# Optimization experiments

Measured on AMD Instinct MI355X. Metric: run time of the kernel, lower is better.

Reference implementation:

```python
import jax, jax.numpy as jnp
import numpy as np

B, T, C = 2, 2048, 2048
N_HEAD, N_KV, HEAD_DIM = 32, 8, 64
REPEATS = N_HEAD // N_KV
WINDOW = 1024
ROPE_BASE = 10000.0


def setup_inputs() -> dict:
    key = jax.random.key(0)
    ks = jax.random.split(key, 5)
    s = 0.02
    return {
        "x": jax.random.normal(ks[0], (B, T, C), jnp.float32),
        "Wq": jax.random.normal(ks[1], (C, N_HEAD * HEAD_DIM), jnp.float32) * s,
        "Wk": jax.random.normal(ks[2], (C, N_KV * HEAD_DIM), jnp.float32) * s,
        "Wv": jax.random.normal(ks[3], (C, N_KV * HEAD_DIM), jnp.float32) * s,
        "Wo": jax.random.normal(ks[4], (N_HEAD * HEAD_DIM, C), jnp.float32) * s,
    }


def _rope(q, k):
    # q: (B,H,T,D), k: (B,Hk,T,D) -- standard rotate-half RoPE
    D = q.shape[-1]
    inv_freq = 1.0 / (ROPE_BASE ** (jnp.arange(0, D, 2, dtype=jnp.float32) / D))
    ang = jnp.arange(q.shape[2], dtype=jnp.float32)[:, None] * inv_freq[None, :]  # (T, D/2)
    cos = jnp.concatenate([jnp.cos(ang), jnp.cos(ang)], axis=-1)  # (T, D)
    sin = jnp.concatenate([jnp.sin(ang), jnp.sin(ang)], axis=-1)

    def rot_half(x):
        x1, x2 = jnp.split(x, 2, axis=-1)
        return jnp.concatenate([-x2, x1], axis=-1)

    def apply(x):
        return x * cos + rot_half(x) * sin

    return apply(q), apply(k)


def reference(x, Wq, Wk, Wv, Wo):
    Bx, Tx, Cx = x.shape
    q = (x @ Wq).reshape(Bx, Tx, N_HEAD, HEAD_DIM).transpose(0, 2, 1, 3)   # (B,H,T,D)
    k = (x @ Wk).reshape(Bx, Tx, N_KV, HEAD_DIM).transpose(0, 2, 1, 3)     # (B,Hk,T,D)
    v = (x @ Wv).reshape(Bx, Tx, N_KV, HEAD_DIM).transpose(0, 2, 1, 3)
    q, k = _rope(q, k)

    # GQA: group queries per kv head instead of repeat_interleave on k/v (same math)
    qg = q.reshape(Bx, N_KV, REPEATS, Tx, HEAD_DIM)
    scale = 1.0 / jnp.sqrt(jnp.float32(HEAD_DIM))
    scores = jnp.einsum('bgrtd,bgsd->bgrts', qg, k) * scale  # (B,Hk,rep,T,T)

    # sliding-window causal mask: attend to j <= i and i - j < WINDOW
    i = jnp.arange(Tx)[:, None]
    j = jnp.arange(Tx)[None, :]
    allowed = (j <= i) & (i - j < WINDOW)
    scores = jnp.where(allowed, scores, -jnp.inf)

    attn = jax.nn.softmax(scores.astype(jnp.float32), axis=-1).astype(q.dtype)
    out = jnp.einsum('bgrts,bgsd->bgrtd', attn, v)            # (B,Hk,rep,T,D)
    out = out.reshape(Bx, N_HEAD, Tx, HEAD_DIM).transpose(0, 2, 1, 3).reshape(Bx, Tx, N_HEAD * HEAD_DIM)
    return out @ Wo
```

## Files before the change

kernel.cpp:

```cpp
#include <hip/hip_runtime.h>

typedef unsigned short u16;
typedef __attribute__((ext_vector_type(8))) unsigned short u16x8;
typedef __attribute__((ext_vector_type(2))) unsigned int u32x2;
typedef __attribute__((ext_vector_type(8))) __bf16 bf16x8;
typedef __attribute__((ext_vector_type(4))) float f32x4;

#define T_SEQ 2048
#define WINDOW 1024
#define QSCALE 0.18033688011112042f

static __device__ __forceinline__ u16 f2bf(float f) {
    unsigned int u = __float_as_uint(f);
    u += 0x7fffu + ((u >> 16) & 1u);
    return (u16)(u >> 16);
}
static __device__ __forceinline__ float bf2f(u16 h) {
    return __uint_as_float(((unsigned int)h) << 16);
}
static __device__ __forceinline__ bf16x8 ld_bf8(const u16* p) {
    return __builtin_bit_cast(bf16x8, *(const u16x8*)p);
}
static __device__ __forceinline__ unsigned int cvt_pk_bf16(float lo, float hi) {
    unsigned int r;
    asm("v_cvt_pk_bf16_f32 %0, %1, %2" : "=v"(r) : "v"(lo), "v"(hi));
    return r;
}
static __device__ __forceinline__ float exp2f_raw(float x) {
#if __has_builtin(__builtin_amdgcn_exp2f)
    return __builtin_amdgcn_exp2f(x);
#else
    return exp2f(x);
#endif
}
static __device__ __forceinline__ void g2l16(const void* g, void* l) {
    __builtin_amdgcn_global_load_lds(
        (const __attribute__((address_space(1))) void*)g,
        (__attribute__((address_space(3))) void*)l, 16, 0, 0);
}

__global__ __launch_bounds__(256)
void rope_tab_kernel(float2* __restrict__ tab)
{
    int idx = blockIdx.x * 256 + threadIdx.x;
    int t = idx >> 5, dp = idx & 31;
    float inv_freq = __expf(-dp * 0.28782313662425574f);
    float ang = (float)t * inv_freq;
    float s, c;
    sincosf(ang, &s, &c);
    tab[idx] = make_float2(c, s);
}

__global__ __launch_bounds__(256)
void convert_x(const float* __restrict__ src, u16* __restrict__ dst)
{
    int i8 = blockIdx.x * 256 + threadIdx.x;
    size_t base = (size_t)i8 * 8;
    float4 a = *(const float4*)(src + base);
    float4 b = *(const float4*)(src + base + 4);
    u16x8 o = { f2bf(a.x), f2bf(a.y), f2bf(a.z), f2bf(a.w),
                f2bf(b.x), f2bf(b.y), f2bf(b.z), f2bf(b.w) };
    *(u16x8*)(dst + base) = o;
}

__global__ __launch_bounds__(256)
void trans_conv_all(const float* __restrict__ Wq, const float* __restrict__ Wk,
                    const float* __restrict__ Wv, const float* __restrict__ Wo,
                    u16* __restrict__ WqkvT, u16* __restrict__ WoT)
{
    __shared__ __align__(16) u16 tile[64][72];
    const int z = blockIdx.z;
    const float* src; int N; float scale; u16* dst;
    if (z == 0)      { src = Wq; N = 2048; scale = QSCALE; dst = WqkvT; }
    else if (z == 1) { src = Wk; N = 512;  scale = 1.f;    dst = WqkvT + (size_t)2048 * 2048; }
    else if (z == 2) { src = Wv; N = 512;  scale = 1.f;    dst = WqkvT + (size_t)2560 * 2048; }
    else             { src = Wo; N = 2048; scale = 1.f;    dst = WoT; }
    if ((int)blockIdx.y * 64 >= N) return;

    const int tid = threadIdx.x;
    const int k0 = blockIdx.x * 64;
    const int n0 = blockIdx.y * 64;
    {
        int r = tid >> 2, c0 = (tid & 3) * 16;
        const float* sp = src + (size_t)(k0 + r) * N + n0 + c0;
        float4 v0 = *(const float4*)(sp + 0);
        float4 v1 = *(const float4*)(sp + 4);
        float4 v2 = *(const float4*)(sp + 8);
        float4 v3 = *(const float4*)(sp + 12);
        u16x8 s0 = { f2bf(v0.x * scale), f2bf(v0.y * scale), f2bf(v0.z * scale), f2bf(v0.w * scale),
                     f2bf(v1.x * scale), f2bf(v1.y * scale), f2bf(v1.z * scale), f2bf(v1.w * scale) };
        u16x8 s1 = { f2bf(v2.x * scale), f2bf(v2.y * scale), f2bf(v2.z * scale), f2bf(v2.w * scale),
                     f2bf(v3.x * scale), f2bf(v3.y * scale), f2bf(v3.z * scale), f2bf(v3.w * scale) };
        *(u16x8*)&tile[r][c0]     = s0;
        *(u16x8*)&tile[r][c0 + 8] = s1;
    }
    __syncthreads();
    {
        int n = tid >> 2, j0 = (tid & 3) * 16;
        u16x8 o0, o1;
        #pragma unroll
        for (int i = 0; i < 8; ++i) o0[i] = tile[j0 + i][n];
        #pragma unroll
        for (int i = 0; i < 8; ++i) o1[i] = tile[j0 + 8 + i][n];
        u16* dp = dst + (size_t)(n0 + n) * 2048 + k0 + j0;
        *(u16x8*)dp       = o0;
        *(u16x8*)(dp + 8) = o1;
    }
}

struct GemmAcc { f32x4 a[8][4]; };

__device__ __forceinline__ void gemm_core_128(const u16* __restrict__ Ag,
                                              const u16* __restrict__ Bg,
                                              u16 (*Al)[64], u16 (*Bl)[64],
                                              int lane, int w, GemmAcc& acc)
{
    const int r8 = lane >> 3;
    const int cs = (lane & 7) ^ r8;
    const u16* ag = Ag + (size_t)(w * 64 + r8) * 2048 + cs * 8;
    const u16* bg = Bg + (size_t)(w * 64 + r8) * 2048 + cs * 8;
    const int fr = lane & 15;
    const int hq = lane >> 4;

    for (int kb = 0; kb < 2048; kb += 64) {
        #pragma unroll
        for (int ii = 0; ii < 8; ++ii)
            g2l16(ag + (size_t)(ii * 8) * 2048 + kb, &Al[w * 64 + ii * 8][0]);
        #pragma unroll
        for (int ii = 0; ii < 8; ++ii)
            g2l16(bg + (size_t)(ii * 8) * 2048 + kb, &Bl[w * 64 + ii * 8][0]);
        __syncthreads();

        #pragma unroll
        for (int kk = 0; kk < 2; ++kk) {
            bf16x8 af[8], bfn[4];
            #pragma unroll
            for (int m = 0; m < 8; ++m) {
                int row = m * 16 + fr;
                int pc = (kk * 4 + hq) ^ (row & 7);
                af[m] = ld_bf8(&Al[row][pc * 8]);
            }
            #pragma unroll
            for (int n = 0; n < 4; ++n) {
                int row = w * 64 + n * 16 + fr;
                int pc = (kk * 4 + hq) ^ (row & 7);
                bfn[n] = ld_bf8(&Bl[row][pc * 8]);
            }
            #pragma unroll
            for (int m = 0; m < 8; ++m)
                #pragma unroll
                for (int n = 0; n < 4; ++n)
                    acc.a[m][n] = __builtin_amdgcn_mfma_f32_16x16x32_bf16(af[m], bfn[n], acc.a[m][n], 0, 0, 0);
        }
        __syncthreads();
    }
}

__global__ __launch_bounds__(128, 2)
void qkv_gemm(const u16* __restrict__ xb, const u16* __restrict__ Wt,
              const float2* __restrict__ tab,
              u16* __restrict__ Qb, u16* __restrict__ Kb, u16* __restrict__ Vb)
{
    __shared__ __align__(16) u16 Al[128][64];
    __shared__ __align__(16) u16 Bl[128][64];
    const int tid = threadIdx.x;
    const int lane = tid & 63;
    const int w = tid >> 6;
    const int m0  = blockIdx.x * 128;
    const int n0g = blockIdx.y * 128;

    GemmAcc acc = {};
    gemm_core_128(xb + (size_t)m0 * 2048, Wt + (size_t)n0g * 2048, Al, Bl, lane, w, acc);

    const int hq = lane >> 4;
    const int c0 = lane & 15;
    const int colbase = n0g + w * 64;
    const bool isV = (n0g >= 2560);
    const bool isQ = (n0g < 2048);

    #pragma unroll
    for (int m = 0; m < 8; ++m) {
        #pragma unroll
        for (int r = 0; r < 4; ++r) {
            int rw = m0 + m * 16 + hq * 4 + r;
            int b = rw >> 11, t = rw & 2047;
            if (!isV) {
                #pragma unroll
                for (int np = 0; np < 2; ++np) {
                    int dp = np * 16 + c0;
                    float2 cs = tab[t * 32 + dp];
                    float x1 = acc.a[m][np][r];
                    float x2 = acc.a[m][np + 2][r];
                    float lo = x1 * cs.x - x2 * cs.y;
                    float hi = x2 * cs.x + x1 * cs.y;
                    if (isQ) {
                        int h = colbase >> 6;
                        size_t base = (((size_t)b * 32 + h) * 2048 + t) * 64 + dp;
                        Qb[base]      = f2bf(lo);
                        Qb[base + 32] = f2bf(hi);
                    } else {
                        int hk = (colbase - 2048) >> 6;
                        size_t base = (((size_t)b * 8 + hk) * 2048 + t) * 64 + dp;
                        Kb[base]      = f2bf(lo);
                        Kb[base + 32] = f2bf(hi);
                    }
                }
            } else {
                #pragma unroll
                for (int n = 0; n < 4; ++n) {
                    int c2 = colbase + n * 16 + c0 - 2560;
                    int hk = c2 >> 6, d = c2 & 63;
                    Vb[(((size_t)b * 8 + hk) * 2048 + t) * 64 + d] = f2bf(acc.a[m][n][r]);
                }
            }
        }
    }
}

__global__ __launch_bounds__(128, 2)
void out_gemm(const u16* __restrict__ A, const u16* __restrict__ Wt, float* __restrict__ C)
{
    __shared__ __align__(16) u16 Al[128][64];
    __shared__ __align__(16) u16 Bl[128][64];
    const int tid = threadIdx.x;
    const int lane = tid & 63;
    const int w = tid >> 6;
    const int m0 = blockIdx.x * 128;
    const int n0 = blockIdx.y * 128;

    GemmAcc acc = {};
    gemm_core_128(A + (size_t)m0 * 2048, Wt + (size_t)n0 * 2048, Al, Bl, lane, w, acc);

    const int hq = lane >> 4;
    const int c0 = lane & 15;
    #pragma unroll
    for (int m = 0; m < 8; ++m) {
        #pragma unroll
        for (int n = 0; n < 4; ++n) {
            #pragma unroll
            for (int r = 0; r < 4; ++r) {
                int rw = m0 + m * 16 + hq * 4 + r;
                int col = n0 + w * 64 + n * 16 + c0;
                C[(size_t)rw * 2048 + col] = acc.a[m][n][r];
            }
        }
    }
}

__global__ __launch_bounds__(256)
void vtrans(const u16* __restrict__ Vb, u16* __restrict__ Vt)
{
    __shared__ __align__(16) u16 tile[64][68];
    const int tid = threadIdx.x;
    const int t0 = blockIdx.x * 64;
    const size_t base = (size_t)blockIdx.y * 2048 * 64;
    {
        int r = tid >> 2, c0 = (tid & 3) * 16;
        const u16* src = Vb + base + (size_t)(t0 + r) * 64 + c0;
        *(u16x8*)&tile[r][c0]     = *(const u16x8*)src;
        *(u16x8*)&tile[r][c0 + 8] = *(const u16x8*)(src + 8);
    }
    __syncthreads();
    {
        int d = tid >> 2, j0 = (tid & 3) * 16;
        u16x8 o0, o1;
        #pragma unroll
        for (int i = 0; i < 8; ++i) o0[i] = tile[j0 + i][d];
        #pragma unroll
        for (int i = 0; i < 8; ++i) o1[i] = tile[j0 + 8 + i][d];
        u16* dst = Vt + base + (size_t)d * 2048 + t0 + j0;
        *(u16x8*)dst       = o0;
        *(u16x8*)(dst + 8) = o1;
    }
}

__global__ __launch_bounds__(256)
void attn_kernel(const u16* __restrict__ Qb, const u16* __restrict__ Kb,
                 const u16* __restrict__ Vt, u16* __restrict__ AO)
{
    __shared__ __align__(16) u16 Kl[64][64];
    __shared__ __align__(16) u16 Vl[64][64];
    __shared__ __align__(16) u16 Pl[4][16][64];

    const int tid = threadIdx.x;
    const int lane = tid & 63;
    const int w = tid >> 6;
    const int q = lane & 15;
    const int hq = lane >> 4;
    const int q0 = blockIdx.x * 64;
    const int bh = blockIdx.y;
    const int b = bh >> 5, h = bh & 31;
    const int hk = h >> 2;
    const size_t qbase  = (size_t)bh * 2048 * 64;
    const size_t kvbase = ((size_t)b * 8 + hk) * 2048 * 64;

    const int sj = tid >> 2;
    const int sd = (tid & 3) * 16;
    const int sc0 = (tid & 3) * 2;
    const int sw0 = ((sc0    ) ^ (sj & 7)) << 3;
    const int sw1 = ((sc0 + 1) ^ (sj & 7)) << 3;
    const int ca0 = ((hq    ) ^ (q & 7)) << 3;
    const int ca1 = ((hq + 4) ^ (q & 7)) << 3;

    bf16x8 qf0, qf1;
    {
        const u16* qp = Qb + qbase + (size_t)(q0 + w * 16 + q) * 64 + hq * 8;
        qf0 = ld_bf8(qp);
        qf1 = ld_bf8(qp + 32);
    }

    float mrun = -1e20f, lrun = 0.f;
    f32x4 o[4] = {};

    int kbeg = q0 - (WINDOW - 1);
    if (kbeg < 0) kbeg = 0;
    kbeg &= ~63;
    const int kend = q0 + 64;

    const int wrow_min = q0 + w * 16;
    const int wrow_max = wrow_min + 15;
    const int iq = wrow_min + q;

    u16x8 kr0, kr1, vr0, vr1;
    {
        const u16* kg = Kb + kvbase + (size_t)(kbeg + sj) * 64 + sd;
        kr0 = *(const u16x8*)kg;
        kr1 = *(const u16x8*)(kg + 8);
        const u16* vg = Vt + kvbase + (size_t)sj * 2048 + kbeg + sd;
        vr0 = *(const u16x8*)vg;
        vr1 = *(const u16x8*)(vg + 8);
    }
    *(u16x8*)&Kl[sj][sw0] = kr0;
    *(u16x8*)&Kl[sj][sw1] = kr1;
    *(u16x8*)&Vl[sj][sw0] = vr0;
    *(u16x8*)&Vl[sj][sw1] = vr1;
    __syncthreads();

    for (int k0 = kbeg; k0 < kend; k0 += 64) {
        const bool has_next = (k0 + 64 < kend);
        if (has_next) {
            const u16* kg = Kb + kvbase + (size_t)(k0 + 64 + sj) * 64 + sd;
            kr0 = *(const u16x8*)kg;
            kr1 = *(const u16x8*)(kg + 8);
            const u16* vg = Vt + kvbase + (size_t)sj * 2048 + k0 + 64 + sd;
            vr0 = *(const u16x8*)vg;
            vr1 = *(const u16x8*)(vg + 8);
        }

        bool active = (k0 <= wrow_max) && (k0 + 63 >= wrow_min - (WINDOW - 1));
        if (active) {
            f32x4 s[4];
            #pragma unroll
            for (int nf = 0; nf < 4; ++nf) {
                bf16x8 kb0 = ld_bf8(&Kl[nf * 16 + q][ca0]);
                bf16x8 kb1 = ld_bf8(&Kl[nf * 16 + q][ca1]);
                f32x4 a = {};
                a = __builtin_amdgcn_mfma_f32_16x16x32_bf16(kb0, qf0, a, 0, 0, 0);
                a = __builtin_amdgcn_mfma_f32_16x16x32_bf16(kb1, qf1, a, 0, 0, 0);
                s[nf] = a;
            }
            bool need_causal = (k0 + 63 > wrow_min);
            bool need_window = (wrow_max - k0) >= WINDOW;
            if (need_causal || need_window) {
                #pragma unroll
                for (int nf = 0; nf < 4; ++nf) {
                    #pragma unroll
                    for (int r = 0; r < 4; ++r) {
                        int j = k0 + nf * 16 + hq * 4 + r;
                        bool ok = (j <= iq) && (iq - j < WINDOW);
                        if (!ok) s[nf][r] = -1e30f;
                    }
                }
            }
            float tmax = s[0][0];
            #pragma unroll
            for (int nf = 0; nf < 4; ++nf)
                #pragma unroll
                for (int r = 0; r < 4; ++r) tmax = fmaxf(tmax, s[nf][r]);
            tmax = fmaxf(tmax, __shfl_xor(tmax, 16));
            tmax = fmaxf(tmax, __shfl_xor(tmax, 32));

            bool skip = __all(tmax <= mrun + 11.5f);
            float mnew = skip ? mrun : fmaxf(mrun, tmax);

            float tsum = 0.f;
            #pragma unroll
            for (int nf = 0; nf < 4; ++nf) {
                float p0 = exp2f_raw(s[nf][0] - mnew);
                float p1 = exp2f_raw(s[nf][1] - mnew);
                float p2 = exp2f_raw(s[nf][2] - mnew);
                float p3 = exp2f_raw(s[nf][3] - mnew);
                tsum += (p0 + p1) + (p2 + p3);
                u32x2 pw = { cvt_pk_bf16(p0, p1), cvt_pk_bf16(p2, p3) };
                int cpw = (((2 * nf + (hq >> 1)) ^ (q & 7)) << 3) + ((hq & 1) << 2);
                *(u32x2*)&Pl[w][q][cpw] = pw;
            }
            tsum += __shfl_xor(tsum, 16);
            tsum += __shfl_xor(tsum, 32);

            if (skip) {
                lrun += tsum;
            } else {
                float sc = exp2f_raw(mrun - mnew);
                mrun = mnew;
                lrun = lrun * sc + tsum;
                float osc[4];
                #pragma unroll
                for (int r = 0; r < 4; ++r)
                    osc[r] = __shfl(sc, (lane & 48) + hq * 4 + r);
                #pragma unroll
                for (int nf = 0; nf < 4; ++nf)
                    #pragma unroll
                    for (int r = 0; r < 4; ++r)
                        o[nf][r] *= osc[r];
            }

            bf16x8 pa0 = ld_bf8(&Pl[w][q][ca0]);
            bf16x8 pa1 = ld_bf8(&Pl[w][q][ca1]);
            #pragma unroll
            for (int nf = 0; nf < 4; ++nf) {
                bf16x8 vb0 = ld_bf8(&Vl[nf * 16 + q][ca0]);
                bf16x8 vb1 = ld_bf8(&Vl[nf * 16 + q][ca1]);
                o[nf] = __builtin_amdgcn_mfma_f32_16x16x32_bf16(pa0, vb0, o[nf], 0, 0, 0);
                o[nf] = __builtin_amdgcn_mfma_f32_16x16x32_bf16(pa1, vb1, o[nf], 0, 0, 0);
            }
        }
        __syncthreads();
        if (has_next) {
            *(u16x8*)&Kl[sj][sw0] = kr0;
            *(u16x8*)&Kl[sj][sw1] = kr1;
            *(u16x8*)&Vl[sj][sw0] = vr0;
            *(u16x8*)&Vl[sj][sw1] = vr1;
        }
        __syncthreads();
    }

    float linv_own = 1.f / lrun;
    float linv[4];
    #pragma unroll
    for (int r = 0; r < 4; ++r)
        linv[r] = __shfl(linv_own, (lane & 48) + hq * 4 + r);
    #pragma unroll
    for (int nf = 0; nf < 4; ++nf) {
        #pragma unroll
        for (int r = 0; r < 4; ++r) {
            int i = q0 + w * 16 + hq * 4 + r;
            int d = nf * 16 + q;
            AO[((size_t)b * 2048 + i) * 2048 + h * 64 + d] = f2bf(o[nf][r] * linv[r]);
        }
    }
}

extern "C" void kernel_launch(void* const* d_in, const int* in_sizes, int n_in,
                              void* d_out, int out_size, void* d_ws, size_t ws_size,
                              hipStream_t stream)
{
    const float* x  = (const float*)d_in[0];
    const float* Wq = (const float*)d_in[1];
    const float* Wk = (const float*)d_in[2];
    const float* Wv = (const float*)d_in[3];
    const float* Wo = (const float*)d_in[4];
    float* out = (float*)d_out;

    u16* Qb    = (u16*)d_ws;
    u16* Kb    = Qb    + (size_t)8388608;
    u16* Vb    = Kb    + (size_t)2097152;
    u16* Vt    = Vb    + (size_t)2097152;
    u16* AO    = Vt    + (size_t)2097152;
    u16* xb    = AO    + (size_t)8388608;
    u16* WqkvT = xb    + (size_t)8388608;
    u16* WoT   = WqkvT + (size_t)6291456;
    float2* tab = (float2*)(WoT + (size_t)4194304);

    rope_tab_kernel<<<256, 256, 0, stream>>>(tab);
    convert_x<<<4096, 256, 0, stream>>>(x, xb);
    trans_conv_all<<<dim3(32, 32, 4), 256, 0, stream>>>(Wq, Wk, Wv, Wo, WqkvT, WoT);

    qkv_gemm<<<dim3(32, 24), 128, 0, stream>>>(xb, WqkvT, tab, Qb, Kb, Vb);
    vtrans<<<dim3(32, 16), 256, 0, stream>>>(Vb, Vt);
    attn_kernel<<<dim3(32, 64), 256, 0, stream>>>(Qb, Kb, Vt, AO);
    out_gemm<<<dim3(32, 16), 128, 0, stream>>>(AO, WoT, out);
}
```

Before: 204.4 us.

## Double attention query tile to 128 rows and schedule heavy blocks first

The attention kernel now uses 512 threads (8 waves) per block covering 128 query rows, so each K/V tile staged in shared memory serves twice as many queries and the number of blocks is halved. The per-thread staging load is reduced to one 16-byte vector for K and one for V. Block order is reversed so the blocks with the latest queries, which have the longest key ranges, are launched first to balance the tail. In exchange, each block covers a wider key range, with some tiles inactive for part of its waves, and occupancy per block is larger.

```diff
diff --git a/kernel.cpp b/kernel.cpp
--- a/kernel.cpp
+++ b/kernel.cpp
@@ -274,31 +274,29 @@
     }
 }
 
-__global__ __launch_bounds__(256)
+__global__ __launch_bounds__(512)
 void attn_kernel(const u16* __restrict__ Qb, const u16* __restrict__ Kb,
                  const u16* __restrict__ Vt, u16* __restrict__ AO)
 {
     __shared__ __align__(16) u16 Kl[64][64];
     __shared__ __align__(16) u16 Vl[64][64];
-    __shared__ __align__(16) u16 Pl[4][16][64];
+    __shared__ __align__(16) u16 Pl[8][16][64];
 
     const int tid = threadIdx.x;
     const int lane = tid & 63;
     const int w = tid >> 6;
     const int q = lane & 15;
     const int hq = lane >> 4;
-    const int q0 = blockIdx.x * 64;
+    const int q0 = (15 - blockIdx.x) * 128;
     const int bh = blockIdx.y;
     const int b = bh >> 5, h = bh & 31;
     const int hk = h >> 2;
     const size_t qbase  = (size_t)bh * 2048 * 64;
     const size_t kvbase = ((size_t)b * 8 + hk) * 2048 * 64;
 
-    const int sj = tid >> 2;
-    const int sd = (tid & 3) * 16;
-    const int sc0 = (tid & 3) * 2;
-    const int sw0 = ((sc0    ) ^ (sj & 7)) << 3;
-    const int sw1 = ((sc0 + 1) ^ (sj & 7)) << 3;
+    const int sj = tid >> 3;
+    const int sc = tid & 7;
+    const int sw = (sc ^ (sj & 7)) << 3;
     const int ca0 = ((hq    ) ^ (q & 7)) << 3;
     const int ca1 = ((hq + 4) ^ (q & 7)) << 3;
 
@@ -315,36 +313,30 @@
     int kbeg = q0 - (WINDOW - 1);
     if (kbeg < 0) kbeg = 0;
     kbeg &= ~63;
-    const int kend = q0 + 64;
+    const int kend = q0 + 128;
 
     const int wrow_min = q0 + w * 16;
     const int wrow_max = wrow_min + 15;
     const int iq = wrow_min + q;
 
-    u16x8 kr0, kr1, vr0, vr1;
-    {
-        const u16* kg = Kb + kvbase + (size_t)(kbeg + sj) * 64 + sd;
-        kr0 = *(const u16x8*)kg;
-        kr1 = *(const u16x8*)(kg + 8);
-        const u16* vg = Vt + kvbase + (size_t)sj * 2048 + kbeg + sd;
-        vr0 = *(const u16x8*)vg;
-        vr1 = *(const u16x8*)(vg + 8);
-    }
-    *(u16x8*)&Kl[sj][sw0] = kr0;
-    *(u16x8*)&Kl[sj][sw1] = kr1;
-    *(u16x8*)&Vl[sj][sw0] = vr0;
-    *(u16x8*)&Vl[sj][sw1] = vr1;
+    u16x8 kr, vr;
+    {
+        const u16* kg = Kb + kvbase + (size_t)(kbeg + sj) * 64 + sc * 8;
+        kr = *(const u16x8*)kg;
+        const u16* vg = Vt + kvbase + (size_t)sj * 2048 + kbeg + sc * 8;
+        vr = *(const u16x8*)vg;
+    }
+    *(u16x8*)&Kl[sj][sw] = kr;
+    *(u16x8*)&Vl[sj][sw] = vr;
     __syncthreads();
 
     for (int k0 = kbeg; k0 < kend; k0 += 64) {
         const bool has_next = (k0 + 64 < kend);
         if (has_next) {
-            const u16* kg = Kb + kvbase + (size_t)(k0 + 64 + sj) * 64 + sd;
-            kr0 = *(const u16x8*)kg;
-            kr1 = *(const u16x8*)(kg + 8);
-            const u16* vg = Vt + kvbase + (size_t)sj * 2048 + k0 + 64 + sd;
-            vr0 = *(const u16x8*)vg;
-            vr1 = *(const u16x8*)(vg + 8);
+            const u16* kg = Kb + kvbase + (size_t)(k0 + 64 + sj) * 64 + sc * 8;
+            kr = *(const u16x8*)kg;
+            const u16* vg = Vt + kvbase + (size_t)sj * 2048 + k0 + 64 + sc * 8;
+            vr = *(const u16x8*)vg;
         }
 
         bool active = (k0 <= wrow_max) && (k0 + 63 >= wrow_min - (WINDOW - 1));
@@ -401,13 +393,13 @@
             if (skip) {
                 lrun += tsum;
             } else {
-                float sc = exp2f_raw(mrun - mnew);
+                float sc2 = exp2f_raw(mrun - mnew);
                 mrun = mnew;
-                lrun = lrun * sc + tsum;
+                lrun = lrun * sc2 + tsum;
                 float osc[4];
                 #pragma unroll
                 for (int r = 0; r < 4; ++r)
-                    osc[r] = __shfl(sc, (lane & 48) + hq * 4 + r);
+                    osc[r] = __shfl(sc2, (lane & 48) + hq * 4 + r);
                 #pragma unroll
                 for (int nf = 0; nf < 4; ++nf)
                     #pragma unroll
@@ -427,10 +419,8 @@
         }
         __syncthreads();
         if (has_next) {
-            *(u16x8*)&Kl[sj][sw0] = kr0;
-            *(u16x8*)&Kl[sj][sw1] = kr1;
-            *(u16x8*)&Vl[sj][sw0] = vr0;
-            *(u16x8*)&Vl[sj][sw1] = vr1;
+            *(u16x8*)&Kl[sj][sw] = kr;
+            *(u16x8*)&Vl[sj][sw] = vr;
         }
         __syncthreads();
     }
@@ -478,6 +468,6 @@
 
     qkv_gemm<<<dim3(32, 24), 128, 0, stream>>>(xb, WqkvT, tab, Qb, Kb, Vb);
     vtrans<<<dim3(32, 16), 256, 0, stream>>>(Vb, Vt);
-    attn_kernel<<<dim3(32, 64), 256, 0, stream>>>(Qb, Kb, Vt, AO);
+    attn_kernel<<<dim3(16, 64), 512, 0, stream>>>(Qb, Kb, Vt, AO);
     out_gemm<<<dim3(32, 16), 128, 0, stream>>>(AO, WoT, out);
 }
```

Result: faster. 198.3 us (median of 2 runs) (-3.0%).
